# Optimization experiments

Measured on AMD Instinct MI355X. Metric: run time of the kernel, lower is better.

## Reference

```python
import jax, jax.numpy as jnp
from jax import lax
import numpy as np

EPS = 1e-08
BETA_VAL = 0.9
B_VAL = 1.0
SIGMA_VAL = 10.0

@jax.custom_vjp
def spike_fn(mthr, sigma):
    # Heaviside forward; SuperSpike surrogate gradient in backward
    return (mthr > 0).astype(mthr.dtype)

def _spike_fwd(mthr, sigma):
    return (mthr > 0).astype(mthr.dtype), (mthr, sigma)

def _spike_bwd(res, g):
    mthr, sigma = res
    grad = g / (sigma * jnp.abs(mthr) + 1.0) ** 2
    return grad, jnp.zeros_like(sigma)

spike_fn.defvjp(_spike_fwd, _spike_bwd)


def setup_inputs() -> dict:
    key = jax.random.key(0)
    kx, kw, kv = jax.random.split(key, 3)
    B, T, I, O = 128, 100, 1024, 1024
    x = jax.random.normal(kx, (B, T, I), dtype=jnp.float32)
    w = (jax.random.normal(kw, (I, O), dtype=jnp.float32)
         * np.float32(np.sqrt(1.0 / I)))  # mean 0, std w_init_std*sqrt(1/I)
    v = (jax.random.normal(kv, (O, O), dtype=jnp.float32)
         * np.float32(np.sqrt(1.0 / O)))
    beta = jnp.full((1,), BETA_VAL, dtype=jnp.float32)   # one_per_layer
    b = jnp.full((O,), B_VAL, dtype=jnp.float32)
    sigma = jnp.full((O,), SIGMA_VAL, dtype=jnp.float32)  # surrogate_sigma_mode='all'
    return {"x": x, "w": w, "v": v, "beta": beta, "b": b, "sigma": sigma}


def reference(x, w, v, beta, b, sigma):
    B, T, I = x.shape
    O = w.shape[1]
    h = jnp.einsum('bti,io->bto', x, w)            # [B,T,O]
    d = jnp.einsum('ai,ao->io', w, w)              # lateral term w^T w, [O,O]
    norm = (w ** 2).sum(0)                         # [O]
    inv_norm = 1.0 / (norm + EPS)

    mem0 = jnp.zeros((B, O), dtype=x.dtype)
    spk0 = jnp.zeros((B, O), dtype=x.dtype)

    def step(carry, h_t):
        mem, spk = carry
        rst = spk @ d                              # lateral reset [B,O]
        inp = h_t + spk @ v                        # recurrent input
        # Leaky neuron, soft reset
        mem = (mem - rst) * beta + inp * (1.0 - beta)
        mthr = mem * inv_norm - b
        spk = spike_fn(mthr, sigma)
        return (mem, spk), spk

    h_t_first = jnp.swapaxes(h, 0, 1)              # [T,B,O]
    _, spk_seq = lax.scan(step, (mem0, spk0), h_t_first)
    spk_rec = jnp.swapaxes(spk_seq, 0, 1)          # [B,T,O]

    loss = 0.5 * (spk_rec ** 2).mean()             # Regularization 'squared'
    spk_spread_loss = spk_rec.sum(axis=(0, 2)).max() / (B * O)  # 'max'
    return spk_rec, loss, spk_spread_loss
```

## Files before the change

kernel.cpp:

```cpp
#include <hip/hip_runtime.h>
#include <cstdint>
#include <cstddef>

#define I_DIM 1024
#define O_DIM 1024
#define B_DIM 128
#define T_DIM 100
#define PANEL 32768
#define QSTep 512

typedef __attribute__((ext_vector_type(8))) __bf16 bf16x8;
typedef __attribute__((ext_vector_type(16))) float f32x16;

__device__ __forceinline__ unsigned short bf16rn(float x) {
  unsigned u = __float_as_uint(x);
  unsigned r = u + 0x7FFFu + ((u >> 16) & 1u);
  return (unsigned short)(r >> 16);
}
__device__ __forceinline__ void split2(float x, unsigned short& h,
                                       unsigned short& l) {
  h = bf16rn(x);
  float hf = __uint_as_float(((unsigned)h) << 16);
  l = bf16rn(x - hf);
}

__global__ __launch_bounds__(256) void prep_kernel(
    const float* __restrict__ w, const float* __restrict__ x,
    unsigned short* __restrict__ wTth, unsigned short* __restrict__ wTtl,
    unsigned short* __restrict__ xth, unsigned short* __restrict__ xtl,
    double* __restrict__ normpart) {
  __shared__ float tile[64][65];
  __shared__ double red[4][64];
  const int id = blockIdx.x;
  const int tid = threadIdx.x;
  if (id < 256) {
    const int a0 = (id >> 4) * 64, o0 = (id & 15) * 64;
    const int tr = tid >> 4, tc4 = (tid & 15) * 4;
#pragma unroll
    for (int rr = 0; rr < 64; rr += 16) {
      float4 v = *(const float4*)&w[(size_t)(a0 + tr + rr) * O_DIM + o0 + tc4];
      tile[tr + rr][tc4 + 0] = v.x;
      tile[tr + rr][tc4 + 1] = v.y;
      tile[tr + rr][tc4 + 2] = v.z;
      tile[tr + rr][tc4 + 3] = v.w;
    }
    __syncthreads();
    {
      const int ol = tid & 63, seg = tid >> 6;
      double s = 0.0;
#pragma unroll
      for (int i = 0; i < 16; ++i) {
        double v = (double)tile[seg * 16 + i][ol];
        s += v * v;
      }
      red[seg][ol] = s;
    }
    const int q = (a0 >> 4) + (tc4 >> 4);
    const int kh = (tc4 >> 3) & 1;
    const int inner = tc4 & 7;
#pragma unroll
    for (int rr = 0; rr < 64; rr += 16) {
      int o = o0 + tr + rr;
      unsigned short hh[4], ll[4];
#pragma unroll
      for (int j = 0; j < 4; ++j) split2(tile[tc4 + j][tr + rr], hh[j], ll[j]);
      int l = (o & 31) + 32 * kh;
      size_t base = ((size_t)(o >> 5) * PANEL) + (size_t)q * QSTep +
                    (size_t)l * 8 + inner;
      *(ushort4*)&wTth[base] = make_ushort4(hh[0], hh[1], hh[2], hh[3]);
      *(ushort4*)&wTtl[base] = make_ushort4(ll[0], ll[1], ll[2], ll[3]);
    }
    __syncthreads();
    if (tid < 64)
      normpart[(size_t)(a0 >> 6) * O_DIM + o0 + tid] =
          red[0][tid] + red[1][tid] + red[2][tid] + red[3][tid];
  } else {
    const int p = (id - 256) >> 2, sub = (id - 256) & 3;
    const int wq = tid >> 6, lane = tid & 63;
    const int row = lane & 31, kh = lane >> 5;
    const float* src = x + (size_t)(p * 32 + row) * I_DIM + kh * 8;
#pragma unroll
    for (int i = sub * 4; i < sub * 4 + 4; ++i) {
      const int q = i * 4 + wq;
      const float* s = src + q * 16;
      float4 v0 = *(const float4*)(s);
      float4 v1 = *(const float4*)(s + 4);
      unsigned short h[8], l[8];
      split2(v0.x, h[0], l[0]);
      split2(v0.y, h[1], l[1]);
      split2(v0.z, h[2], l[2]);
      split2(v0.w, h[3], l[3]);
      split2(v1.x, h[4], l[4]);
      split2(v1.y, h[5], l[5]);
      split2(v1.z, h[6], l[6]);
      split2(v1.w, h[7], l[7]);
      size_t base = ((size_t)p * PANEL) + (size_t)q * QSTep + (size_t)lane * 8;
      *(ushort4*)&xth[base] = make_ushort4(h[0], h[1], h[2], h[3]);
      *(ushort4*)&xth[base + 4] = make_ushort4(h[4], h[5], h[6], h[7]);
      *(ushort4*)&xtl[base] = make_ushort4(l[0], l[1], l[2], l[3]);
      *(ushort4*)&xtl[base + 4] = make_ushort4(l[4], l[5], l[6], l[7]);
    }
  }
}

__global__ __launch_bounds__(256, 3) void gemm_fused(
    const unsigned short* __restrict__ xth,
    const unsigned short* __restrict__ xtl,
    const unsigned short* __restrict__ wTth,
    const unsigned short* __restrict__ wTtl, const float* __restrict__ v,
    const float* __restrict__ beta_p, float* __restrict__ h,
    float* __restrict__ M) {
  const int id = blockIdx.x;
  const int tid = threadIdx.x;
  const int wv = tid >> 6, lane = tid & 63;
  const int wm = wv >> 1, wn = wv & 1;
  const int lm = lane & 31, lkh = lane >> 5;
  const bool is_h = id < 800;
  int rbase, cbase;
  const unsigned short *Ah_src, *Al_src;
  if (is_h) {
    rbase = (id % 100) * 128;
    cbase = (id / 100) * 128;
    Ah_src = xth;
    Al_src = xtl;
  } else {
    rbase = ((id - 800) >> 3) * 128;
    cbase = ((id - 800) & 7) * 128;
    Ah_src = wTth;
    Al_src = wTtl;
  }
  f32x16 acc[2][2];
#pragma unroll
  for (int a = 0; a < 2; ++a)
#pragma unroll
    for (int b = 0; b < 2; ++b)
#pragma unroll
      for (int e = 0; e < 16; ++e) acc[a][b][e] = 0.f;
  const unsigned short *pah[2], *pal[2], *pbh[2], *pbl[2];
#pragma unroll
  for (int t = 0; t < 2; ++t) {
    size_t offA =
        ((size_t)((rbase >> 5) + wm * 2 + t) * PANEL) + (size_t)lane * 8;
    size_t offB =
        ((size_t)((cbase >> 5) + wn * 2 + t) * PANEL) + (size_t)lane * 8;
    pah[t] = Ah_src + offA;
    pal[t] = Al_src + offA;
    pbh[t] = wTth + offB;
    pbl[t] = wTtl + offB;
  }
  bf16x8 fah[2][2], fal[2][2], fbh[2][2], fbl[2][2];
#pragma unroll
  for (int t = 0; t < 2; ++t) {
    fah[0][t] = *(const bf16x8*)(pah[t]);
    fal[0][t] = *(const bf16x8*)(pal[t]);
    fbh[0][t] = *(const bf16x8*)(pbh[t]);
    fbl[0][t] = *(const bf16x8*)(pbl[t]);
  }
#pragma unroll 2
  for (int q = 0; q < 64; ++q) {
    const int cb = q & 1;
    if (q < 63) {
      size_t d = (size_t)(q + 1) * QSTep;
#pragma unroll
      for (int t = 0; t < 2; ++t) {
        fah[cb ^ 1][t] = *(const bf16x8*)(pah[t] + d);
        fal[cb ^ 1][t] = *(const bf16x8*)(pal[t] + d);
        fbh[cb ^ 1][t] = *(const bf16x8*)(pbh[t] + d);
        fbl[cb ^ 1][t] = *(const bf16x8*)(pbl[t] + d);
      }
    }
#pragma unroll
    for (int mt = 0; mt < 2; ++mt)
#pragma unroll
      for (int nt = 0; nt < 2; ++nt)
        acc[mt][nt] = __builtin_amdgcn_mfma_f32_32x32x16_bf16(
            fah[cb][mt], fbh[cb][nt], acc[mt][nt], 0, 0, 0);
#pragma unroll
    for (int mt = 0; mt < 2; ++mt)
#pragma unroll
      for (int nt = 0; nt < 2; ++nt)
        acc[mt][nt] = __builtin_amdgcn_mfma_f32_32x32x16_bf16(
            fah[cb][mt], fbl[cb][nt], acc[mt][nt], 0, 0, 0);
#pragma unroll
    for (int mt = 0; mt < 2; ++mt)
#pragma unroll
      for (int nt = 0; nt < 2; ++nt)
        acc[mt][nt] = __builtin_amdgcn_mfma_f32_32x32x16_bf16(
            fal[cb][mt], fbh[cb][nt], acc[mt][nt], 0, 0, 0);
  }
  if (is_h) {
#pragma unroll
    for (int mt = 0; mt < 2; ++mt)
#pragma unroll
      for (int nt = 0; nt < 2; ++nt) {
        int col = cbase + wn * 64 + nt * 32 + lm;
#pragma unroll
        for (int r = 0; r < 16; ++r) {
          int row =
              rbase + wm * 64 + mt * 32 + (r & 3) + 8 * (r >> 2) + 4 * lkh;
          h[(size_t)row * O_DIM + col] = acc[mt][nt][r];
        }
      }
  } else {
    const float beta = beta_p[0];
    const float ombeta = 1.0f - beta;
#pragma unroll
    for (int mt = 0; mt < 2; ++mt)
#pragma unroll
      for (int nt = 0; nt < 2; ++nt) {
        int col = cbase + wn * 64 + nt * 32 + lm;
#pragma unroll
        for (int r = 0; r < 16; ++r) {
          int row =
              rbase + wm * 64 + mt * 32 + (r & 3) + 8 * (r >> 2) + 4 * lkh;
          M[(size_t)row * O_DIM + col] =
              ombeta * v[(size_t)row * O_DIM + col] - beta * acc[mt][nt][r];
        }
      }
  }
}

__global__ __launch_bounds__(64) void scan_kernel(
    const float* __restrict__ h, const float* __restrict__ M,
    const double* __restrict__ normpart, const float* __restrict__ bvec,
    const float* __restrict__ beta_p, float* __restrict__ out,
    int* __restrict__ wgcnt, int* __restrict__ done) {
  const int b = blockIdx.x, lane = threadIdx.x;
  const double beta = (double)beta_p[0];
  const double ombeta = 1.0 - beta;
  double mem[4][4], inv[4][4], bth[4][4];
  unsigned long long pmask[4][4];
#pragma unroll
  for (int k = 0; k < 4; ++k)
#pragma unroll
    for (int j = 0; j < 4; ++j) {
      const int o = 256 * k + 4 * lane + j;
      mem[k][j] = 0.0;
      double s = 0.0;
#pragma unroll
      for (int g = 0; g < 16; ++g) s += normpart[(size_t)g * O_DIM + o];
      inv[k][j] = 1.0 / (s + 1e-8);
      bth[k][j] = (double)bvec[o];
      pmask[k][j] = 0ull;
    }
  const float* hb = h + (size_t)b * T_DIM * O_DIM;
  float* obp = out + (size_t)b * T_DIM * O_DIM;
  float4 hv0[4], hv1[4];
#pragma unroll
  for (int k = 0; k < 4; ++k) {
    hv0[k] = *(const float4*)&hb[256 * k + 4 * lane];
    hv1[k] = *(const float4*)&hb[O_DIM + 256 * k + 4 * lane];
  }
  int total = 0;
  for (int t = 0; t < T_DIM; ++t) {
    float4 hv2[4];
#pragma unroll
    for (int k = 0; k < 4; ++k) hv2[k] = make_float4(0.f, 0.f, 0.f, 0.f);
    if (t + 2 < T_DIM) {
#pragma unroll
      for (int k = 0; k < 4; ++k)
        hv2[k] = *(const float4*)&hb[(size_t)(t + 2) * O_DIM + 256 * k +
                                     4 * lane];
    }
    double lat[4][4] = {};
#pragma unroll
    for (int k2 = 0; k2 < 4; ++k2)
#pragma unroll
      for (int j2 = 0; j2 < 4; ++j2) {
        unsigned long long m = pmask[k2][j2];
        while (m) {
          const int p = (int)__builtin_ctzll(m);
          m &= m - 1;
          const int i = 256 * k2 + 4 * p + j2;
          const float* Mr = M + (size_t)i * O_DIM + 4 * lane;
#pragma unroll
          for (int k = 0; k < 4; ++k) {
            float4 mv = *(const float4*)(Mr + 256 * k);
            lat[k][0] += (double)mv.x;
            lat[k][1] += (double)mv.y;
            lat[k][2] += (double)mv.z;
            lat[k][3] += (double)mv.w;
          }
        }
      }
    int cnt = 0;
#pragma unroll
    for (int k = 0; k < 4; ++k) {
      const float hvv[4] = {hv0[k].x, hv0[k].y, hv0[k].z, hv0[k].w};
      float os[4];
#pragma unroll
      for (int j = 0; j < 4; ++j) {
        mem[k][j] = mem[k][j] * beta + (double)hvv[j] * ombeta + lat[k][j];
        double mthr = mem[k][j] * inv[k][j] - bth[k][j];
        bool s = mthr > 0.0;
        os[j] = s ? 1.0f : 0.0f;
        unsigned long long mk = __ballot(s);
        pmask[k][j] = mk;
        cnt += (int)__popcll(mk);
      }
      *(float4*)&obp[(size_t)t * O_DIM + 256 * k + 4 * lane] =
          make_float4(os[0], os[1], os[2], os[3]);
      hv0[k] = hv1[k];
      hv1[k] = hv2[k];
    }
    total += 0;
    if (lane == 0) wgcnt[b * T_DIM + t] = cnt;
  }
  __threadfence();
  int old = 0;
  if (lane == 0) old = atomicAdd(done, 1);
  old = __shfl(old, 0, 64);
  if (old == B_DIM - 1) {
    __threadfence();
    long long tsum = 0;
    int mx = 0;
    for (int t = lane; t < T_DIM; t += 64) {
      int st = 0;
      for (int bb = 0; bb < B_DIM; ++bb) st += wgcnt[bb * T_DIM + t];
      tsum += st;
      if (st > mx) mx = st;
    }
#pragma unroll
    for (int off = 32; off > 0; off >>= 1) {
      tsum += __shfl_down((long long)tsum, off, 64);
      int m2 = __shfl_down(mx, off, 64);
      if (m2 > mx) mx = m2;
    }
    if (lane == 0) {
      const double N = (double)B_DIM * T_DIM * O_DIM;
      out[(size_t)B_DIM * T_DIM * O_DIM] = (float)(0.5 * (double)tsum / N);
      out[(size_t)B_DIM * T_DIM * O_DIM + 1] =
          (float)((double)mx / (double)(B_DIM * O_DIM));
    }
  }
}

extern "C" void kernel_launch(void* const* d_in, const int* in_sizes, int n_in,
                              void* d_out, int out_size, void* d_ws,
                              size_t ws_size, hipStream_t stream) {
  const float* x = (const float*)d_in[0];
  const float* w = (const float*)d_in[1];
  const float* v = (const float*)d_in[2];
  const float* beta = (const float*)d_in[3];
  const float* b = (const float*)d_in[4];
  float* out = (float*)d_out;

  char* ws = (char*)d_ws;
  const size_t OFF_M = 0;
  const size_t OFF_H = 4194304;
  const size_t OFF_WTH = 56623104;
  const size_t OFF_WTL = 58720256;
  const size_t OFF_NP = 60817408;
  const size_t OFF_DONE = 60948480;
  const size_t OFF_XTH = 60948992;
  const size_t OFF_XTL = 87163392;
  float* M = (float*)(ws + OFF_M);
  float* h = (float*)(ws + OFF_H);
  unsigned short* wTth = (unsigned short*)(ws + OFF_WTH);
  unsigned short* wTtl = (unsigned short*)(ws + OFF_WTL);
  double* normpart = (double*)(ws + OFF_NP);
  int* done = (int*)(ws + OFF_DONE);
  unsigned short* xth = (unsigned short*)(ws + OFF_XTH);
  unsigned short* xtl = (unsigned short*)(ws + OFF_XTL);
  int* wgcnt = (int*)(ws + OFF_XTH);

  hipMemsetAsync(done, 0, 512, stream);
  hipLaunchKernelGGL(prep_kernel, dim3(1856), dim3(256), 0, stream, w, x, wTth,
                     wTtl, xth, xtl, normpart);
  hipLaunchKernelGGL(gemm_fused, dim3(864), dim3(256), 0, stream, xth, xtl,
                     wTth, wTtl, v, beta, h, M);
  hipLaunchKernelGGL(scan_kernel, dim3(128), dim3(64), 0, stream, h, M,
                     normpart, b, beta, out, wgcnt, done);
}
```

Baseline: 315.1 us.

## Fuse prep and GEMM into one cooperative kernel with a grid sync

```diff
diff --git a/kernel.cpp b/kernel.cpp
--- a/kernel.cpp
+++ b/kernel.cpp
@@ -1,4 +1,5 @@
 #include <hip/hip_runtime.h>
+#include <hip/hip_cooperative_groups.h>
 #include <cstdint>
 #include <cstddef>
 
@@ -8,6 +9,9 @@
 #define T_DIM 100
 #define PANEL 32768
 #define QSTep 512
+#define NCOOP 512
+
+namespace cg = cooperative_groups;
 
 typedef __attribute__((ext_vector_type(8))) __bf16 bf16x8;
 typedef __attribute__((ext_vector_type(16))) float f32x16;
@@ -24,25 +28,21 @@
   l = bf16rn(x - hf);
 }
 
-__global__ __launch_bounds__(256) void prep_kernel(
-    const float* __restrict__ w, const float* __restrict__ x,
+__device__ __forceinline__ void prep_unit(
+    int u, int tid, const float* __restrict__ w, const float* __restrict__ x,
     unsigned short* __restrict__ wTth, unsigned short* __restrict__ wTtl,
     unsigned short* __restrict__ xth, unsigned short* __restrict__ xtl,
-    double* __restrict__ normpart) {
-  __shared__ float tile[64][65];
-  __shared__ double red[4][64];
-  const int id = blockIdx.x;
-  const int tid = threadIdx.x;
-  if (id < 256) {
-    const int a0 = (id >> 4) * 64, o0 = (id & 15) * 64;
+    double* __restrict__ normpart, float (*tile)[65], double (*red)[64]) {
+  if (u < 256) {
+    const int a0 = (u >> 4) * 64, o0 = (u & 15) * 64;
     const int tr = tid >> 4, tc4 = (tid & 15) * 4;
 #pragma unroll
     for (int rr = 0; rr < 64; rr += 16) {
-      float4 v = *(const float4*)&w[(size_t)(a0 + tr + rr) * O_DIM + o0 + tc4];
-      tile[tr + rr][tc4 + 0] = v.x;
-      tile[tr + rr][tc4 + 1] = v.y;
-      tile[tr + rr][tc4 + 2] = v.z;
-      tile[tr + rr][tc4 + 3] = v.w;
+      float4 vv = *(const float4*)&w[(size_t)(a0 + tr + rr) * O_DIM + o0 + tc4];
+      tile[tr + rr][tc4 + 0] = vv.x;
+      tile[tr + rr][tc4 + 1] = vv.y;
+      tile[tr + rr][tc4 + 2] = vv.z;
+      tile[tr + rr][tc4 + 3] = vv.w;
     }
     __syncthreads();
     {
@@ -50,8 +50,8 @@
       double s = 0.0;
 #pragma unroll
       for (int i = 0; i < 16; ++i) {
-        double v = (double)tile[seg * 16 + i][ol];
-        s += v * v;
+        double vv = (double)tile[seg * 16 + i][ol];
+        s += vv * vv;
       }
       red[seg][ol] = s;
     }
@@ -75,7 +75,7 @@
       normpart[(size_t)(a0 >> 6) * O_DIM + o0 + tid] =
           red[0][tid] + red[1][tid] + red[2][tid] + red[3][tid];
   } else {
-    const int p = (id - 256) >> 2, sub = (id - 256) & 3;
+    const int p = (u - 256) >> 2, sub = (u - 256) & 3;
     const int wq = tid >> 6, lane = tid & 63;
     const int row = lane & 31, kh = lane >> 5;
     const float* src = x + (size_t)(p * 32 + row) * I_DIM + kh * 8;
@@ -85,33 +85,31 @@
       const float* s = src + q * 16;
       float4 v0 = *(const float4*)(s);
       float4 v1 = *(const float4*)(s + 4);
-      unsigned short h[8], l[8];
-      split2(v0.x, h[0], l[0]);
-      split2(v0.y, h[1], l[1]);
-      split2(v0.z, h[2], l[2]);
-      split2(v0.w, h[3], l[3]);
-      split2(v1.x, h[4], l[4]);
-      split2(v1.y, h[5], l[5]);
-      split2(v1.z, h[6], l[6]);
-      split2(v1.w, h[7], l[7]);
+      unsigned short hh[8], ll[8];
+      split2(v0.x, hh[0], ll[0]);
+      split2(v0.y, hh[1], ll[1]);
+      split2(v0.z, hh[2], ll[2]);
+      split2(v0.w, hh[3], ll[3]);
+      split2(v1.x, hh[4], ll[4]);
+      split2(v1.y, hh[5], ll[5]);
+      split2(v1.z, hh[6], ll[6]);
+      split2(v1.w, hh[7], ll[7]);
       size_t base = ((size_t)p * PANEL) + (size_t)q * QSTep + (size_t)lane * 8;
-      *(ushort4*)&xth[base] = make_ushort4(h[0], h[1], h[2], h[3]);
-      *(ushort4*)&xth[base + 4] = make_ushort4(h[4], h[5], h[6], h[7]);
-      *(ushort4*)&xtl[base] = make_ushort4(l[0], l[1], l[2], l[3]);
-      *(ushort4*)&xtl[base + 4] = make_ushort4(l[4], l[5], l[6], l[7]);
-    }
-  }
-}
-
-__global__ __launch_bounds__(256, 3) void gemm_fused(
-    const unsigned short* __restrict__ xth,
+      *(ushort4*)&xth[base] = make_ushort4(hh[0], hh[1], hh[2], hh[3]);
+      *(ushort4*)&xth[base + 4] = make_ushort4(hh[4], hh[5], hh[6], hh[7]);
+      *(ushort4*)&xtl[base] = make_ushort4(ll[0], ll[1], ll[2], ll[3]);
+      *(ushort4*)&xtl[base + 4] = make_ushort4(ll[4], ll[5], ll[6], ll[7]);
+    }
+  }
+}
+
+__device__ __forceinline__ void gemm_unit(
+    int id, int tid, const unsigned short* __restrict__ xth,
     const unsigned short* __restrict__ xtl,
     const unsigned short* __restrict__ wTth,
     const unsigned short* __restrict__ wTtl, const float* __restrict__ v,
     const float* __restrict__ beta_p, float* __restrict__ h,
     float* __restrict__ M) {
-  const int id = blockIdx.x;
-  const int tid = threadIdx.x;
   const int wv = tid >> 6, lane = tid & 63;
   const int wm = wv >> 1, wn = wv & 1;
   const int lm = lane & 31, lkh = lane >> 5;
@@ -220,6 +218,48 @@
   }
 }
 
+__global__ __launch_bounds__(256, 2) void fused_kernel(
+    const float* __restrict__ w, const float* __restrict__ x,
+    unsigned short* __restrict__ wTth, unsigned short* __restrict__ wTtl,
+    unsigned short* __restrict__ xth, unsigned short* __restrict__ xtl,
+    double* __restrict__ normpart, const float* __restrict__ v,
+    const float* __restrict__ beta_p, float* __restrict__ h,
+    float* __restrict__ M, int* __restrict__ done) {
+  __shared__ float tile[64][65];
+  __shared__ double red[4][64];
+  const int tid = threadIdx.x;
+  if (blockIdx.x == 0 && tid == 0) *done = 0;
+  for (int u = blockIdx.x; u < 1856; u += NCOOP)
+    prep_unit(u, tid, w, x, wTth, wTtl, xth, xtl, normpart, tile, red);
+  __threadfence();
+  cg::this_grid().sync();
+  __threadfence();
+  for (int id = blockIdx.x; id < 864; id += NCOOP)
+    gemm_unit(id, tid, xth, xtl, wTth, wTtl, v, beta_p, h, M);
+}
+
+__global__ __launch_bounds__(256) void prep_kernel(
+    const float* __restrict__ w, const float* __restrict__ x,
+    unsigned short* __restrict__ wTth, unsigned short* __restrict__ wTtl,
+    unsigned short* __restrict__ xth, unsigned short* __restrict__ xtl,
+    double* __restrict__ normpart, int* __restrict__ done) {
+  __shared__ float tile[64][65];
+  __shared__ double red[4][64];
+  if (blockIdx.x == 0 && threadIdx.x == 0) *done = 0;
+  prep_unit(blockIdx.x, threadIdx.x, w, x, wTth, wTtl, xth, xtl, normpart,
+            tile, red);
+}
+
+__global__ __launch_bounds__(256, 3) void gemm_kernel(
+    const unsigned short* __restrict__ xth,
+    const unsigned short* __restrict__ xtl,
+    const unsigned short* __restrict__ wTth,
+    const unsigned short* __restrict__ wTtl, const float* __restrict__ v,
+    const float* __restrict__ beta_p, float* __restrict__ h,
+    float* __restrict__ M) {
+  gemm_unit(blockIdx.x, threadIdx.x, xth, xtl, wTth, wTtl, v, beta_p, h, M);
+}
+
 __global__ __launch_bounds__(64) void scan_kernel(
     const float* __restrict__ h, const float* __restrict__ M,
     const double* __restrict__ normpart, const float* __restrict__ bvec,
@@ -228,7 +268,7 @@
   const int b = blockIdx.x, lane = threadIdx.x;
   const double beta = (double)beta_p[0];
   const double ombeta = 1.0 - beta;
-  double mem[4][4], inv[4][4], bth[4][4];
+  double mem[4][4], thr[4][4];
   unsigned long long pmask[4][4];
 #pragma unroll
   for (int k = 0; k < 4; ++k)
@@ -239,8 +279,7 @@
       double s = 0.0;
 #pragma unroll
       for (int g = 0; g < 16; ++g) s += normpart[(size_t)g * O_DIM + o];
-      inv[k][j] = 1.0 / (s + 1e-8);
-      bth[k][j] = (double)bvec[o];
+      thr[k][j] = (s + 1e-8) * (double)bvec[o];
       pmask[k][j] = 0ull;
     }
   const float* hb = h + (size_t)b * T_DIM * O_DIM;
@@ -251,7 +290,6 @@
     hv0[k] = *(const float4*)&hb[256 * k + 4 * lane];
     hv1[k] = *(const float4*)&hb[O_DIM + 256 * k + 4 * lane];
   }
-  int total = 0;
   for (int t = 0; t < T_DIM; ++t) {
     float4 hv2[4];
 #pragma unroll
@@ -259,8 +297,8 @@
     if (t + 2 < T_DIM) {
 #pragma unroll
       for (int k = 0; k < 4; ++k)
-        hv2[k] = *(const float4*)&hb[(size_t)(t + 2) * O_DIM + 256 * k +
-                                     4 * lane];
+        hv2[k] =
+            *(const float4*)&hb[(size_t)(t + 2) * O_DIM + 256 * k + 4 * lane];
     }
     double lat[4][4] = {};
 #pragma unroll
@@ -291,8 +329,7 @@
 #pragma unroll
       for (int j = 0; j < 4; ++j) {
         mem[k][j] = mem[k][j] * beta + (double)hvv[j] * ombeta + lat[k][j];
-        double mthr = mem[k][j] * inv[k][j] - bth[k][j];
-        bool s = mthr > 0.0;
+        bool s = mem[k][j] > thr[k][j];
         os[j] = s ? 1.0f : 0.0f;
         unsigned long long mk = __ballot(s);
         pmask[k][j] = mk;
@@ -303,7 +340,6 @@
       hv0[k] = hv1[k];
       hv1[k] = hv2[k];
     }
-    total += 0;
     if (lane == 0) wgcnt[b * T_DIM + t] = cnt;
   }
   __threadfence();
@@ -364,11 +400,21 @@
   unsigned short* xtl = (unsigned short*)(ws + OFF_XTL);
   int* wgcnt = (int*)(ws + OFF_XTH);
 
-  hipMemsetAsync(done, 0, 512, stream);
-  hipLaunchKernelGGL(prep_kernel, dim3(1856), dim3(256), 0, stream, w, x, wTth,
-                     wTtl, xth, xtl, normpart);
-  hipLaunchKernelGGL(gemm_fused, dim3(864), dim3(256), 0, stream, xth, xtl,
-                     wTth, wTtl, v, beta, h, M);
+  const float* wp = w;
+  const float* xp = x;
+  const float* vp = v;
+  const float* bp = beta;
+  void* args[] = {(void*)&wp,   (void*)&xp,  (void*)&wTth,     (void*)&wTtl,
+                  (void*)&xth,  (void*)&xtl, (void*)&normpart, (void*)&vp,
+                  (void*)&bp,   (void*)&h,   (void*)&M,        (void*)&done};
+  hipError_t err = hipLaunchCooperativeKernel(
+      (const void*)fused_kernel, dim3(NCOOP), dim3(256), args, 0, stream);
+  if (err != hipSuccess) {
+    hipLaunchKernelGGL(prep_kernel, dim3(1856), dim3(256), 0, stream, w, x,
+                       wTth, wTtl, xth, xtl, normpart, done);
+    hipLaunchKernelGGL(gemm_kernel, dim3(864), dim3(256), 0, stream, xth, xtl,
+                       wTth, wTtl, v, beta, h, M);
+  }
   hipLaunchKernelGGL(scan_kernel, dim3(128), dim3(64), 0, stream, h, M,
                      normpart, b, beta, out, wgcnt, done);
 }
```

After: 470.7 us. 1.49x slower.
